# Kernel optimization log

Measured on AMD Instinct MI355X. Metric: run time of the kernel, lower is better.

## Reference

```python
import jax, jax.numpy as jnp
import numpy as np

DIM = 384
WIN = 64
HEADS = 12
B_ = 4096


def setup_inputs() -> dict:
    key = jax.random.key(0)
    k1, k2, k3, k4, k5 = jax.random.split(key, 5)
    x = jax.random.normal(k1, (B_, WIN, DIM), dtype=jnp.float32)
    # torch Linear weights: qkv.weight [3*dim, dim], proj.weight [dim, dim], proj.bias [dim]
    qkv_w = jax.random.normal(k2, (3 * DIM, DIM), dtype=jnp.float32) * (DIM ** -0.5)
    proj_w = jax.random.normal(k3, (DIM, DIM), dtype=jnp.float32) * (DIM ** -0.5)
    proj_b = jax.random.normal(k4, (DIM,), dtype=jnp.float32) * 0.02
    bias_table = jax.random.normal(k5, (2 * WIN - 1, HEADS), dtype=jnp.float32) * 0.02
    return {"x": x, "qkv_w": qkv_w, "proj_w": proj_w, "proj_b": proj_b,
            "bias_table": bias_table}


def reference(x, qkv_w, proj_w, proj_b, bias_table):
    B, N, C = x.shape
    H = HEADS
    hd = C // H
    scale = hd ** -0.5
    # qkv projection (torch: x @ W.T), split into q,k,v [B,H,N,hd]
    qkv = jnp.einsum('bnc,dc->bnd', x, qkv_w)
    qkv = qkv.reshape(B, N, 3, H, hd).transpose(2, 0, 3, 1, 4)
    q, k, v = qkv[0] * scale, qkv[1], qkv[2]
    attn = jnp.einsum('bhnd,bhmd->bhnm', q, k)  # [B,H,N,N]
    # relative position bias: index [N,N] into table [2W-1,H]
    coords = jnp.arange(N)
    rel_idx = coords[:, None] - coords[None, :] + (N - 1)  # [N,N]
    bias = bias_table[rel_idx]  # [N,N,H]
    attn = attn + bias.transpose(2, 0, 1)[None]
    attn = jax.nn.softmax(attn, axis=-1)
    out = jnp.einsum('bhnm,bhmd->bhnd', attn, v)
    out = out.transpose(0, 2, 1, 3).reshape(B, N, C)
    out = jnp.einsum('bnc,dc->bnd', out, proj_w) + proj_b
    return out
```

## Files before the change

### kernel.cpp

```cpp
#include <hip/hip_runtime.h>
#include <stdint.h>

#define DIM 384
#define WIN 64
#define HEADS 12
#define HD 32
#define NWIN 4096

typedef _Float16 f16;
typedef unsigned int u32;
typedef _Float16 half8 __attribute__((ext_vector_type(8)));
typedef _Float16 half4 __attribute__((ext_vector_type(4)));
typedef float floatx4 __attribute__((ext_vector_type(4)));

#define AS1 __attribute__((address_space(1)))
#define AS3 __attribute__((address_space(3)))

__device__ __forceinline__ void gl_lds16(const void* g, void* l) {
    __builtin_amdgcn_global_load_lds((const AS1 u32*)g, (AS3 u32*)l, 16, 0, 0);
}

__global__ void cvt_kernel(const float* __restrict__ in, f16* __restrict__ out, long n4) {
    long i = (long)blockIdx.x * blockDim.x + threadIdx.x;
    const long stride = (long)gridDim.x * blockDim.x;
    for (; i < n4; i += stride) {
        float4 v = ((const float4*)in)[i];
        half4 h;
        h[0] = (f16)v.x; h[1] = (f16)v.y; h[2] = (f16)v.z; h[3] = (f16)v.w;
        ((half4*)out)[i] = h;
    }
}

__global__ void pack_w_kernel(const float* __restrict__ w, f16* __restrict__ Bp) {
    const int t = blockIdx.x * 256 + threadIdx.x;
    const int colb = t / 6144;
    const int r1 = t % 6144;
    const int s = r1 / 512;
    const int r2 = r1 % 512;
    const int kc = r2 >> 7, u = r2 & 127;
    const float* sp = w + (size_t)(colb * 128 + u) * DIM + s * 32 + kc * 8;
    float4 a = *(const float4*)sp;
    float4 b = *(const float4*)(sp + 4);
    half8 o;
    o[0] = (f16)a.x; o[1] = (f16)a.y; o[2] = (f16)a.z; o[3] = (f16)a.w;
    o[4] = (f16)b.x; o[5] = (f16)b.y; o[6] = (f16)b.z; o[7] = (f16)b.w;
    *(half8*)(Bp + (size_t)t * 8) = o;
}

__global__ void pack_x_kernel(const float* __restrict__ x, f16* __restrict__ Xp) {
    const int b = blockIdx.x;
    const int s = b % 12;
    const int rowb = b / 12;
    const int t = threadIdx.x;
    const int kc = t & 3, rr = t >> 2;
#pragma unroll
    for (int h = 0; h < 2; ++h) {
        const int row = rr + h * 64;
        const float* sp = x + (size_t)(rowb * 128 + row) * DIM + s * 32 + kc * 8;
        float4 a = *(const float4*)sp;
        float4 bq = *(const float4*)(sp + 4);
        half8 o;
        o[0] = (f16)a.x;  o[1] = (f16)a.y;  o[2] = (f16)a.z;  o[3] = (f16)a.w;
        o[4] = (f16)bq.x; o[5] = (f16)bq.y; o[6] = (f16)bq.z; o[7] = (f16)bq.w;
        *(half8*)(Xp + ((size_t)b * 512 + kc * 128 + row) * 8) = o;
    }
}

__global__ void qkv_kernel(const f16* __restrict__ Xp, const f16* __restrict__ Bp,
                           f16* __restrict__ q_arr, f16* __restrict__ k_arr,
                           f16* __restrict__ v_int, int nwg)
{
    __shared__ __align__(16) f16 ldsA[3][4096];
    __shared__ __align__(16) f16 ldsB[3][4096];

    int lin = blockIdx.x;
    int nlin = lin;
    if ((nwg & 7) == 0) nlin = (lin & 7) * (nwg >> 3) + (lin >> 3);
    const int colb = nlin % 9, rowb = nlin / 9;

    const int tid = threadIdx.x;
    const int wave = tid >> 6, lane = tid & 63;
    const int g = lane >> 4, c = lane & 15;
    const int wm = wave >> 1, wn = wave & 1;

    floatx4 acc[4][4] = {};

    auto stage = [&](int t) {
        const f16* sa = Xp + (size_t)(rowb * 12 + t) * 4096;
        const f16* sb = Bp + (size_t)(colb * 12 + t) * 4096;
        f16* da = &ldsA[t % 3][0];
        f16* db = &ldsB[t % 3][0];
#pragma unroll
        for (int r = 0; r < 2; ++r) {
            const int ch = r * 256 + tid;
            gl_lds16(sa + (size_t)ch * 8, da + (size_t)ch * 8);
            gl_lds16(sb + (size_t)ch * 8, db + (size_t)ch * 8);
        }
    };

    stage(0); stage(1);

#pragma unroll
    for (int s = 0; s < 12; ++s) {
        if (s < 11) asm volatile("s_waitcnt vmcnt(4)" ::: "memory");
        else        asm volatile("s_waitcnt vmcnt(0)" ::: "memory");
        __builtin_amdgcn_sched_barrier(0);
        __builtin_amdgcn_s_barrier();
        __builtin_amdgcn_sched_barrier(0);
        if (s < 10) stage(s + 2);

        half8 af[4], bf[4];
#pragma unroll
        for (int i = 0; i < 4; ++i) {
            af[i] = *(const half8*)&ldsA[s % 3][g * 1024 + (wm * 64 + i * 16 + c) * 8];
            bf[i] = *(const half8*)&ldsB[s % 3][g * 1024 + (wn * 64 + i * 16 + c) * 8];
        }
#pragma unroll
        for (int mi = 0; mi < 4; ++mi)
#pragma unroll
            for (int ni = 0; ni < 4; ++ni)
                acc[mi][ni] = __builtin_amdgcn_mfma_f32_16x16x32_f16(
                    af[mi], bf[ni], acc[mi][ni], 0, 0, 0);
    }

    const int col0 = colb * 128;
    const int which = colb / 3;
    const int dbase = col0 - which * DIM;
    const int b0 = rowb * 2 + wm;
    if (which < 2) {
        f16* dst = which ? k_arr : q_arr;
        const float sc = which ? 1.0f : 0.17677669529663687f;
#pragma unroll
        for (int ni = 0; ni < 4; ++ni) {
            const int d = dbase + wn * 64 + ni * 16 + c;
            const int h = d >> 5, e = d & 31;
            f16* base = dst + (size_t)(b0 * HEADS + h) * (WIN * HD) + e;
#pragma unroll
            for (int mi = 0; mi < 4; ++mi)
#pragma unroll
                for (int j = 0; j < 4; ++j) {
                    const int n = mi * 16 + g * 4 + j;
                    base[(size_t)n * HD] = (f16)(acc[mi][ni][j] * sc);
                }
        }
    } else {
#pragma unroll
        for (int ni = 0; ni < 4; ++ni) {
            const int d = dbase + wn * 64 + ni * 16 + c;
            const int h = d >> 5, e = d & 31;
            f16* vb = v_int + (size_t)(b0 * HEADS + h) * (WIN * HD);
#pragma unroll
            for (int mi = 0; mi < 4; ++mi) {
                const int n0 = mi * 16 + g * 4;
                half4 pk;
#pragma unroll
                for (int j = 0; j < 4; ++j) pk[j] = (f16)acc[mi][ni][j];
                *(half4*)(vb + (n0 >> 3) * 256 + e * 8 + (n0 & 7)) = pk;
            }
        }
    }
}

__global__ void proj_kernel(const f16* __restrict__ A, const f16* __restrict__ Bw,
                            float* __restrict__ outp, const float* __restrict__ proj_b,
                            int nwg)
{
    __shared__ __align__(16) f16 lds[3][2][4][128][8];

    int lin = blockIdx.x;
    int nlin = lin;
    if ((nwg & 7) == 0) nlin = (lin & 7) * (nwg >> 3) + (lin >> 3);
    const int colb = nlin % 3, rowb = nlin / 3;
    const int col0 = colb * 128, row0 = rowb * 128;

    const int tid = threadIdx.x;
    const int wave = tid >> 6, lane = tid & 63;
    const int g = lane >> 4, c = lane & 15;
    const int wm = wave >> 1, wn = wave & 1;

    floatx4 acc[4][4] = {};

    auto stage = [&](int t) {
        const int k0 = t * 32;
#pragma unroll
        for (int r = 0; r < 4; ++r) {
            const int u = wave + r * 4;
            const int isB = u >> 3;
            const int uu = u & 7;
            const int kc = uu >> 1, m0 = (uu & 1) * 64;
            const f16* src = (isB ? Bw + (size_t)(col0 + m0 + lane) * DIM
                                  : A  + (size_t)(row0 + m0 + lane) * DIM)
                             + k0 + kc * 8;
            gl_lds16(src, &lds[t % 3][isB][kc][m0][0]);
        }
    };

    stage(0); stage(1);

#pragma unroll
    for (int s = 0; s < 12; ++s) {
        if (s < 11) asm volatile("s_waitcnt vmcnt(4)" ::: "memory");
        else        asm volatile("s_waitcnt vmcnt(0)" ::: "memory");
        asm volatile("s_waitcnt lgkmcnt(0)" ::: "memory");
        __builtin_amdgcn_sched_barrier(0);
        __builtin_amdgcn_s_barrier();
        __builtin_amdgcn_sched_barrier(0);
        if (s < 10) stage(s + 2);

        half8 af[4], bf[4];
#pragma unroll
        for (int i = 0; i < 4; ++i) {
            af[i] = *(const half8*)&lds[s % 3][0][g][wm * 64 + i * 16 + c][0];
            bf[i] = *(const half8*)&lds[s % 3][1][g][wn * 64 + i * 16 + c][0];
        }
#pragma unroll
        for (int mi = 0; mi < 4; ++mi)
#pragma unroll
            for (int ni = 0; ni < 4; ++ni)
                acc[mi][ni] = __builtin_amdgcn_mfma_f32_16x16x32_f16(
                    af[mi], bf[ni], acc[mi][ni], 0, 0, 0);
    }

#pragma unroll
    for (int ni = 0; ni < 4; ++ni) {
        const int d = col0 + wn * 64 + ni * 16 + c;
        const float pb = proj_b[d];
#pragma unroll
        for (int mi = 0; mi < 4; ++mi)
#pragma unroll
            for (int j = 0; j < 4; ++j) {
                const size_t trow = (size_t)row0 + wm * 64 + mi * 16 + g * 4 + j;
                outp[trow * DIM + d] = acc[mi][ni][j] + pb;
            }
    }
}

__global__ void attn_kernel(const f16* __restrict__ q_arr, const f16* __restrict__ k_arr,
                            const f16* __restrict__ v_int,
                            const float* __restrict__ bias_table,
                            f16* __restrict__ attn_out)
{
    const int bid = blockIdx.x;
    const int bw = bid / HEADS, h = bid % HEADS;
    const f16* q = q_arr + (size_t)bid * (WIN * HD);
    const f16* k = k_arr + (size_t)bid * (WIN * HD);
    const f16* v = v_int + (size_t)bid * (WIN * HD);

    const int tid = threadIdx.x;
    const int w = tid >> 6, lane = tid & 63;
    const int g = lane >> 4, c = lane & 15;

    __shared__ float bias_lds[2 * WIN - 1];
    __shared__ __align__(16) f16 p_lds[8][64][8];

    for (int i = tid; i < 2 * WIN - 1; i += 256)
        bias_lds[i] = bias_table[(size_t)i * HEADS + h];
    __syncthreads();

    half8 qa = *(const half8*)(q + (16 * w + c) * HD + g * 8);
    floatx4 s[4];
#pragma unroll
    for (int t = 0; t < 4; ++t) {
        half8 kb = *(const half8*)(k + (16 * t + c) * HD + g * 8);
        floatx4 z = {};
        s[t] = __builtin_amdgcn_mfma_f32_16x16x32_f16(qa, kb, z, 0, 0, 0);
    }

    float pr[4][4];
#pragma unroll
    for (int j = 0; j < 4; ++j) {
        const int n = 16 * w + g * 4 + j;
        float mx = -1e30f;
#pragma unroll
        for (int t = 0; t < 4; ++t) {
            const int m = 16 * t + c;
            pr[j][t] = s[t][j] + bias_lds[n - m + 63];
            mx = fmaxf(mx, pr[j][t]);
        }
        mx = fmaxf(mx, __shfl_xor(mx, 1));
        mx = fmaxf(mx, __shfl_xor(mx, 2));
        mx = fmaxf(mx, __shfl_xor(mx, 4));
        mx = fmaxf(mx, __shfl_xor(mx, 8));
        float sum = 0.f;
#pragma unroll
        for (int t = 0; t < 4; ++t) { pr[j][t] = __expf(pr[j][t] - mx); sum += pr[j][t]; }
        sum += __shfl_xor(sum, 1);
        sum += __shfl_xor(sum, 2);
        sum += __shfl_xor(sum, 4);
        sum += __shfl_xor(sum, 8);
        const float r = 1.0f / sum;
#pragma unroll
        for (int t = 0; t < 4; ++t) {
            const int m = 16 * t + c;
            p_lds[m >> 3][n][m & 7] = (f16)(pr[j][t] * r);
        }
    }
    __syncthreads();

    half8 pa0 = *(const half8*)&p_lds[g][16 * w + c][0];
    half8 pa1 = *(const half8*)&p_lds[4 + g][16 * w + c][0];
    floatx4 o[2];
#pragma unroll
    for (int t = 0; t < 2; ++t) {
        half8 vb0 = *(const half8*)(v + g * 256 + (16 * t + c) * 8);
        half8 vb1 = *(const half8*)(v + (4 + g) * 256 + (16 * t + c) * 8);
        floatx4 z = {};
        o[t] = __builtin_amdgcn_mfma_f32_16x16x32_f16(pa0, vb0, z, 0, 0, 0);
        o[t] = __builtin_amdgcn_mfma_f32_16x16x32_f16(pa1, vb1, o[t], 0, 0, 0);
    }
#pragma unroll
    for (int t = 0; t < 2; ++t)
#pragma unroll
        for (int j = 0; j < 4; ++j) {
            const int n = 16 * w + g * 4 + j;
            attn_out[((size_t)bw * WIN + n) * DIM + h * HD + 16 * t + c] = (f16)o[t][j];
        }
}

extern "C" void kernel_launch(void* const* d_in, const int* in_sizes, int n_in,
                              void* d_out, int out_size, void* d_ws, size_t ws_size,
                              hipStream_t stream) {
    const float* x          = (const float*)d_in[0];
    const float* qkv_w      = (const float*)d_in[1];
    const float* proj_w     = (const float*)d_in[2];
    const float* proj_b     = (const float*)d_in[3];
    const float* bias_table = (const float*)d_in[4];
    float* out = (float*)d_out;
    (void)in_sizes; (void)n_in; (void)out_size;

    uintptr_t p = (uintptr_t)d_ws;
    auto carve = [&](size_t bytes) -> void* {
        uintptr_t q = p; p += (bytes + 255) & ~(size_t)255; return (void*)q;
    };
    f16* w16_proj = (f16*)carve((size_t)DIM * DIM * 2);
    f16* Bp       = (f16*)carve((size_t)9 * 12 * 512 * 8 * 2);
    const size_t fixed = p - (uintptr_t)d_ws;

    int CB = NWIN;
    while (CB > 16 && fixed + (size_t)CB * 245760 + 4096 > ws_size) CB >>= 1;

    f16* Xp = (f16*)carve((size_t)CB * WIN * DIM * 2);
    f16* qa = (f16*)carve((size_t)CB * HEADS * WIN * HD * 2);
    f16* ka = (f16*)carve((size_t)CB * HEADS * WIN * HD * 2);
    f16* vi = (f16*)carve((size_t)CB * HEADS * WIN * HD * 2);
    f16* ao = (f16*)carve((size_t)CB * WIN * DIM * 2);

    cvt_kernel<<<dim3(64), dim3(256), 0, stream>>>(proj_w, w16_proj, (long)(DIM * DIM / 4));
    pack_w_kernel<<<dim3(216), dim3(256), 0, stream>>>(qkv_w, Bp);

    for (int c0 = 0; c0 < NWIN; c0 += CB) {
        const float* xc = x + (size_t)c0 * WIN * DIM;
        const int rowbs = CB / 2;

        pack_x_kernel<<<dim3(rowbs * 12), dim3(256), 0, stream>>>(xc, Xp);

        const int nwg1 = rowbs * 9;
        qkv_kernel<<<dim3(nwg1), dim3(256), 0, stream>>>(Xp, Bp, qa, ka, vi, nwg1);

        attn_kernel<<<dim3(CB * HEADS), dim3(256), 0, stream>>>(qa, ka, vi, bias_table, ao);

        const int nwg2 = rowbs * 3;
        proj_kernel<<<dim3(nwg2), dim3(256), 0, stream>>>(ao, w16_proj,
                                                          out + (size_t)c0 * WIN * DIM, proj_b, nwg2);
    }
}
```

Baseline: 917.8 us.

## Enlarge QKV GEMM tile to 256x128 with 512 threads and interleaved staging

The QKV projection kernel moves from a 128x128 tile with 256 threads to a 256x128 tile with 512 threads and a 64-wide K step. Global-to-LDS loads for future stages are interleaved between half-steps, with barriers, waitcnts and setprio around the MFMA blocks. The aim is better reuse of the weight tile and tighter overlap of loads with matrix math. In exchange it uses more LDS (about 144KB) and allows one block per CU, which lowers occupancy. The epilogue indexing is updated for the new row blocking.

After: 990.3 us. 1.08x slower.

```diff
diff --git a/kernel.cpp b/kernel.cpp
--- a/kernel.cpp
+++ b/kernel.cpp
@@ -66,12 +66,13 @@
     }
 }
 
-__global__ void qkv_kernel(const f16* __restrict__ Xp, const f16* __restrict__ Bp,
-                           f16* __restrict__ q_arr, f16* __restrict__ k_arr,
-                           f16* __restrict__ v_int, int nwg)
+__global__ void __launch_bounds__(512, 1)
+qkv_kernel(const f16* __restrict__ Xp, const f16* __restrict__ Bp,
+           f16* __restrict__ q_arr, f16* __restrict__ k_arr,
+           f16* __restrict__ v_int, int nwg)
 {
-    __shared__ __align__(16) f16 ldsA[3][4096];
-    __shared__ __align__(16) f16 ldsB[3][4096];
+    __shared__ __align__(16) f16 ldsA[3][16384];
+    __shared__ __align__(16) f16 ldsB[3][8192];
 
     int lin = blockIdx.x;
     int nlin = lin;
@@ -85,48 +86,68 @@
 
     floatx4 acc[4][4] = {};
 
-    auto stage = [&](int t) {
-        const f16* sa = Xp + (size_t)(rowb * 12 + t) * 4096;
-        const f16* sb = Bp + (size_t)(colb * 12 + t) * 4096;
-        f16* da = &ldsA[t % 3][0];
-        f16* db = &ldsB[t % 3][0];
-#pragma unroll
-        for (int r = 0; r < 2; ++r) {
-            const int ch = r * 256 + tid;
-            gl_lds16(sa + (size_t)ch * 8, da + (size_t)ch * 8);
-            gl_lds16(sb + (size_t)ch * 8, db + (size_t)ch * 8);
-        }
+    auto stA = [&](int t, int r) {
+        const int rh = r >> 1, sh = r & 1;
+        const f16* src = Xp + ((size_t)(2 * rowb + rh) * 12 + (2 * t + sh)) * 4096
+                         + (size_t)tid * 8;
+        gl_lds16(src, &ldsA[t % 3][r * 4096 + tid * 8]);
     };
-
-    stage(0); stage(1);
-
-#pragma unroll
-    for (int s = 0; s < 12; ++s) {
-        if (s < 11) asm volatile("s_waitcnt vmcnt(4)" ::: "memory");
-        else        asm volatile("s_waitcnt vmcnt(0)" ::: "memory");
-        __builtin_amdgcn_sched_barrier(0);
-        __builtin_amdgcn_s_barrier();
-        __builtin_amdgcn_sched_barrier(0);
-        if (s < 10) stage(s + 2);
-
-        half8 af[4], bf[4];
-#pragma unroll
-        for (int i = 0; i < 4; ++i) {
-            af[i] = *(const half8*)&ldsA[s % 3][g * 1024 + (wm * 64 + i * 16 + c) * 8];
-            bf[i] = *(const half8*)&ldsB[s % 3][g * 1024 + (wn * 64 + i * 16 + c) * 8];
-        }
-#pragma unroll
-        for (int mi = 0; mi < 4; ++mi)
-#pragma unroll
-            for (int ni = 0; ni < 4; ++ni)
-                acc[mi][ni] = __builtin_amdgcn_mfma_f32_16x16x32_f16(
-                    af[mi], bf[ni], acc[mi][ni], 0, 0, 0);
-    }
-
-    const int col0 = colb * 128;
+    auto stB = [&](int t, int sh) {
+        const f16* src = Bp + ((size_t)colb * 12 + (2 * t + sh)) * 4096 + (size_t)tid * 8;
+        gl_lds16(src, &ldsB[t % 3][sh * 4096 + tid * 8]);
+    };
+
+    stA(0, 0); stA(0, 1); stA(0, 2); stA(0, 3); stB(0, 0); stB(0, 1);
+    stA(1, 0); stA(1, 1); stA(1, 2); stA(1, 3); stB(1, 0); stB(1, 1);
+    asm volatile("s_waitcnt vmcnt(6)" ::: "memory");
+    __builtin_amdgcn_sched_barrier(0);
+    __builtin_amdgcn_s_barrier();
+    __builtin_amdgcn_sched_barrier(0);
+
+#pragma unroll
+    for (int t = 0; t < 6; ++t) {
+        const f16* ab = &ldsA[t % 3][0];
+        const f16* bb = &ldsB[t % 3][0];
+#pragma unroll
+        for (int sh = 0; sh < 2; ++sh) {
+            half8 af[4], bf[4];
+#pragma unroll
+            for (int mi = 0; mi < 4; ++mi) {
+                const int row = wm * 64 + mi * 16 + c;
+                af[mi] = *(const half8*)(ab + ((row >> 7) * 2 + sh) * 4096
+                                         + g * 1024 + (row & 127) * 8);
+            }
+#pragma unroll
+            for (int ni = 0; ni < 4; ++ni) {
+                const int u = wn * 64 + ni * 16 + c;
+                bf[ni] = *(const half8*)(bb + sh * 4096 + g * 1024 + u * 8);
+            }
+            if (t < 4) {
+                if (sh == 0) { stA(t + 2, 0); stA(t + 2, 1); stA(t + 2, 2); }
+                else         { stA(t + 2, 3); stB(t + 2, 0); stB(t + 2, 1); }
+            }
+            __builtin_amdgcn_s_barrier();
+            __builtin_amdgcn_sched_barrier(0);
+            asm volatile("s_waitcnt lgkmcnt(0)" ::: "memory");
+            __builtin_amdgcn_sched_barrier(0);
+            __builtin_amdgcn_s_setprio(1);
+#pragma unroll
+            for (int mi = 0; mi < 4; ++mi)
+#pragma unroll
+                for (int ni = 0; ni < 4; ++ni)
+                    acc[mi][ni] = __builtin_amdgcn_mfma_f32_16x16x32_f16(
+                        af[mi], bf[ni], acc[mi][ni], 0, 0, 0);
+            __builtin_amdgcn_s_setprio(0);
+            if (sh == 1 && t < 4) asm volatile("s_waitcnt vmcnt(6)" ::: "memory");
+            if (sh == 1 && t == 4) asm volatile("s_waitcnt vmcnt(0)" ::: "memory");
+            __builtin_amdgcn_s_barrier();
+            __builtin_amdgcn_sched_barrier(0);
+        }
+    }
+
     const int which = colb / 3;
-    const int dbase = col0 - which * DIM;
-    const int b0 = rowb * 2 + wm;
+    const int dbase = (colb % 3) * 128;
+    const int b0 = rowb * 4 + wm;
     if (which < 2) {
         f16* dst = which ? k_arr : q_arr;
         const float sc = which ? 1.0f : 0.17677669529663687f;
@@ -354,8 +375,8 @@
 
         pack_x_kernel<<<dim3(rowbs * 12), dim3(256), 0, stream>>>(xc, Xp);
 
-        const int nwg1 = rowbs * 9;
-        qkv_kernel<<<dim3(nwg1), dim3(256), 0, stream>>>(Xp, Bp, qa, ka, vi, nwg1);
+        const int nwg1 = (CB * WIN / 256) * 9;
+        qkv_kernel<<<dim3(nwg1), dim3(512), 0, stream>>>(Xp, Bp, qa, ka, vi, nwg1);
 
         attn_kernel<<<dim3(CB * HEADS), dim3(256), 0, stream>>>(qa, ka, vi, bias_table, ao);
 
```
